# Performance work log

Hardware: AMD Instinct MI355X
Metric: run time of the kernel (lower is better)

The kernel has to match this reference:

```python
import jax, jax.numpy as jnp
import numpy as np

N = 4096   # out_features (rows of W)
M = 4096   # in_features (cols of W)
S_L = 2048 # Givens pairs on rows
S_R = 2048 # Givens pairs on cols
T = 8192   # tokens (batch*seq)
EPS = 1e-6


def _disjoint_pairs(key, n_feat, n_pairs):
    perm = jax.random.permutation(key, n_feat)[: 2 * n_pairs]
    return perm.reshape(n_pairs, 2).astype(jnp.int32)


def setup_inputs() -> dict:
    key = jax.random.key(0)
    ks = jax.random.split(key, 8)
    x = jax.random.normal(ks[0], (T, M), dtype=jnp.float32)
    W = 0.02 * jax.random.normal(ks[1], (N, M), dtype=jnp.float32)
    bias = jnp.zeros((N,), dtype=jnp.float32)
    theta_L = 0.002 * jax.random.normal(ks[2], (S_L,), dtype=jnp.float32)
    theta_R = 0.002 * jax.random.normal(ks[3], (S_R,), dtype=jnp.float32)
    pairs_L = _disjoint_pairs(ks[4], N, S_L)
    pairs_R = _disjoint_pairs(ks[5], M, S_R)
    ecd_log_mag = jnp.zeros((N,), dtype=jnp.float32)
    base_row_norms = jnp.linalg.norm(W, axis=1)  # [N], captured at init
    return {"x": x, "W": W, "bias": bias, "theta_L": theta_L,
            "theta_R": theta_R, "ecd_log_mag": ecd_log_mag,
            "base_row_norms": base_row_norms, "pairs_L": pairs_L,
            "pairs_R": pairs_R}


def _rotate_rows(Wm, pairs, theta):
    # Disjoint Givens rotations on rows: gather pair rows, 2x2 rotate, scatter.
    i, j = pairs[:, 0], pairs[:, 1]
    c = jnp.cos(theta)[:, None]
    s = jnp.sin(theta)[:, None]
    ri, rj = Wm[i], Wm[j]              # [S, M] gathers
    return Wm.at[i].set(c * ri - s * rj).at[j].set(s * ri + c * rj)


def _rotate_cols(Wm, pairs, theta):
    i, j = pairs[:, 0], pairs[:, 1]
    c = jnp.cos(theta)[None, :]
    s = jnp.sin(theta)[None, :]
    ci, cj = Wm[:, i], Wm[:, j]        # [N, S] gathers
    return Wm.at[:, i].set(c * ci - s * cj).at[:, j].set(s * ci + c * cj)


def reference(x, W, bias, theta_L, theta_R, ecd_log_mag, base_row_norms,
              pairs_L, pairs_R):
    # Effective weight: W_eff = G_L(theta_L) @ W @ G_R(theta_R)^T
    W_eff = _rotate_rows(_rotate_cols(W, pairs_R, theta_R), pairs_L, theta_L)
    # Magnitude (ECD) rescaling: restore base per-row norms modulated by
    # learned log-magnitudes.
    row_norms = jnp.sqrt(jnp.sum(W_eff * W_eff, axis=1) + EPS)  # [N]
    scale = base_row_norms * jnp.exp(ecd_log_mag) / row_norms   # [N]
    W_eff = W_eff * scale[:, None]
    return x @ W_eff.T + bias
```

## Files before the change

### kernel.cpp

```cpp
#include <hip/hip_runtime.h>
#include <cstdint>
#include <cstddef>

constexpr int T_N = 8192;
constexpr int MM  = 4096;
constexpr int NN  = 4096;
constexpr int S_L = 2048;
constexpr int S_R = 2048;
constexpr float EPS_ = 1e-6f;

typedef float  f32x4  __attribute__((ext_vector_type(4)));
typedef __bf16 bf16x8 __attribute__((ext_vector_type(8)));
typedef unsigned short ushort8 __attribute__((ext_vector_type(8)));

__device__ __forceinline__ unsigned short f2bf(float f) {
  unsigned int u = __float_as_uint(f);
  u += 0x7FFFu + ((u >> 16) & 1u);
  return (unsigned short)(u >> 16);
}

__global__ void init_maps(float* rowC, float* rowS, int* rowP,
                          float* colC, float* colS, int* colP) {
  int i = blockIdx.x * blockDim.x + threadIdx.x;
  if (i < NN) { rowC[i] = 1.f; rowS[i] = 0.f; rowP[i] = i; }
  if (i < MM) { colC[i] = 1.f; colS[i] = 0.f; colP[i] = i; }
}

__global__ void build_maps(const float* __restrict__ thL, const float* __restrict__ thR,
                           const int* __restrict__ prL, const int* __restrict__ prR,
                           float* rowC, float* rowS, int* rowP,
                           float* colC, float* colS, int* colP) {
  int s = blockIdx.x * blockDim.x + threadIdx.x;
  if (s < S_L) {
    int i = prL[2*s], j = prL[2*s+1];
    float c = cosf(thL[s]), sn = sinf(thL[s]);
    rowC[i] = c; rowS[i] = -sn; rowP[i] = j;
    rowC[j] = c; rowS[j] =  sn; rowP[j] = i;
  }
  if (s < S_R) {
    int i = prR[2*s], j = prR[2*s+1];
    float c = cosf(thR[s]), sn = sinf(thR[s]);
    colC[i] = c; colS[i] = -sn; colP[i] = j;
    colC[j] = c; colS[j] =  sn; colP[j] = i;
  }
}

__global__ __launch_bounds__(256) void build_weff(
    const float* __restrict__ W, const float* __restrict__ brn, const float* __restrict__ elm,
    const float* __restrict__ rowC, const float* __restrict__ rowS, const int* __restrict__ rowP,
    const float* __restrict__ colC, const float* __restrict__ colS, const int* __restrict__ colP,
    unsigned short* __restrict__ Wb)
{
  __shared__ __align__(16) float rA[MM];
  __shared__ __align__(16) float rB[MM];
  __shared__ __align__(16) float rE[MM];
  __shared__ float red[4];

  int n   = blockIdx.x;
  int tid = threadIdx.x;
  int pn  = rowP[n];
  float cl = rowC[n], sl = rowS[n];
  const float* Wn = W + (size_t)n  * MM;
  const float* Wp = W + (size_t)pn * MM;

  for (int m = tid * 4; m < MM; m += 1024) {
    *(f32x4*)&rA[m] = *(const f32x4*)&Wn[m];
    *(f32x4*)&rB[m] = *(const f32x4*)&Wp[m];
  }
  __syncthreads();

  float ss = 0.f;
  for (int m = tid; m < MM; m += 256) {
    int p = colP[m];
    float c = colC[m], s = colS[m];
    float e = cl * (c * rA[m] + s * rA[p]) + sl * (c * rB[m] + s * rB[p]);
    rE[m] = e;
    ss += e * e;
  }
  #pragma unroll
  for (int o = 32; o; o >>= 1) ss += __shfl_xor(ss, o);
  int lane = tid & 63, wid = tid >> 6;
  if (lane == 0) red[wid] = ss;
  __syncthreads();
  float tot = red[0] + red[1] + red[2] + red[3];
  float scale = brn[n] * expf(elm[n]) / sqrtf(tot + EPS_);

  for (int m = tid * 8; m < MM; m += 2048) {
    ushort8 pkt;
    #pragma unroll
    for (int q = 0; q < 8; q++) pkt[q] = f2bf(rE[m + q] * scale);
    *(ushort8*)&Wb[(size_t)n * MM + m] = pkt;
  }
}

__global__ __launch_bounds__(256) void conv_x(const float* __restrict__ x,
                                              unsigned short* __restrict__ xb) {
  const size_t total = (size_t)T_N * MM / 8;
  for (size_t i = (size_t)blockIdx.x * 256 + threadIdx.x; i < total; i += 2048ull * 256ull) {
    const float* s = x + i * 8;
    f32x4 v0 = *(const f32x4*)s;
    f32x4 v1 = *(const f32x4*)(s + 4);
    ushort8 p;
    p[0] = f2bf(v0.x); p[1] = f2bf(v0.y); p[2] = f2bf(v0.z); p[3] = f2bf(v0.w);
    p[4] = f2bf(v1.x); p[5] = f2bf(v1.y); p[6] = f2bf(v1.z); p[7] = f2bf(v1.w);
    *(ushort8*)(xb + i * 8) = p;
  }
}

typedef const __attribute__((address_space(1))) unsigned int* as1_u32p;
typedef __attribute__((address_space(3))) unsigned int* as3_u32p;

__device__ __forceinline__ void gl_lds16(const void* g, void* l) {
  __builtin_amdgcn_global_load_lds((as1_u32p)g, (as3_u32p)l, 16, 0, 0);
}

constexpr int GBM = 256, GBN = 256, GBK = 64;
constexpr int NT = MM / GBK;
constexpr int TILE_BYTES = GBM * GBK * 2;

#define LGKM(N) do { asm volatile("s_waitcnt lgkmcnt(" #N ")" ::: "memory"); \
                     __builtin_amdgcn_sched_barrier(0); } while (0)
#define VMC0()  asm volatile("s_waitcnt vmcnt(0)" ::: "memory")

#define RD_A(DST, AB, Q)                                                      \
  _Pragma("unroll") for (int i_ = 0; i_ < 2; ++i_)                            \
  _Pragma("unroll") for (int kk_ = 0; kk_ < 2; ++kk_)                         \
    DST[i_][kk_] = *(const bf16x8*)((AB) + arow0 + ((Q)*2 + i_) * 2048        \
                                     + ((kk_*64 + lg*16) ^ sw));

#define RD_B(DST, BB)                                                         \
  _Pragma("unroll") for (int ni_ = 0; ni_ < 4; ++ni_)                         \
  _Pragma("unroll") for (int kk_ = 0; kk_ < 2; ++kk_)                         \
    DST[ni_][kk_] = *(const bf16x8*)((BB) + brow0 + ni_ * 2048                \
                                     + ((kk_*64 + lg*16) ^ sw));

#define MFMA_PH(AF, BF, MI0)                                                  \
  __builtin_amdgcn_s_setprio(1);                                              \
  _Pragma("unroll") for (int kk_ = 0; kk_ < 2; ++kk_)                         \
  _Pragma("unroll") for (int i_ = 0; i_ < 2; ++i_)                            \
  _Pragma("unroll") for (int ni_ = 0; ni_ < 4; ++ni_)                         \
    acc[(MI0)+i_][ni_] = __builtin_amdgcn_mfma_f32_16x16x32_bf16(             \
        AF[i_][kk_], BF[ni_][kk_], acc[(MI0)+i_][ni_], 0, 0, 0);              \
  __builtin_amdgcn_s_setprio(0);

#define STAGE(T1)                                                             \
  { const int kof_ = (T1) * GBK;                                              \
    char* dA_ = ldsA + ((T1) & 1) * TILE_BYTES;                               \
    char* dB_ = ldsB + ((T1) & 1) * TILE_BYTES;                               \
    _Pragma("unroll") for (int l_ = 0; l_ < 4; ++l_) {                        \
      gl_lds16(sA + (size_t)l_ * (64 * MM) + kof_, dA_ + dstb + l_ * 8192);   \
      gl_lds16(sB + (size_t)l_ * (64 * MM) + kof_, dB_ + dstb + l_ * 8192);   \
    } }

#define TILE_FULL(T, BFC, BFN, AF0C, AF0N)                                    \
  {                                                                           \
    const int t_ = (T);                                                       \
    const char* Ab_  = ldsA + (t_ & 1) * TILE_BYTES;                          \
    const char* AbN_ = ldsA + ((t_ + 1) & 1) * TILE_BYTES;                    \
    const char* BbN_ = ldsB + ((t_ + 1) & 1) * TILE_BYTES;                    \
    __builtin_amdgcn_s_barrier();                                             \
    STAGE(t_ + 1);                                                            \
    bf16x8 af1[2][2], af2[2][2], af3[2][2];                                   \
    RD_A(af1, Ab_, 1);                                                        \
    LGKM(4);                                                                  \
    MFMA_PH(AF0C, BFC, 0);                                                    \
    RD_A(af2, Ab_, 2);                                                        \
    LGKM(4);                                                                  \
    MFMA_PH(af1, BFC, 2);                                                     \
    RD_A(af3, Ab_, 3);                                                        \
    VMC0();                                                                   \
    __builtin_amdgcn_s_barrier();                                             \
    RD_B(BFN, BbN_);                                                          \
    LGKM(12);                                                                 \
    MFMA_PH(af2, BFC, 4);                                                     \
    RD_A(AF0N, AbN_, 0);                                                      \
    LGKM(12);                                                                 \
    MFMA_PH(af3, BFC, 6);                                                     \
  }

__global__ __launch_bounds__(512, 2) void gemm8(
    const unsigned short* __restrict__ xb,
    const unsigned short* __restrict__ wb,
    const float* __restrict__ bias,
    float* __restrict__ C)
{
  __shared__ __align__(16) unsigned short As[2 * GBM * GBK];
  __shared__ __align__(16) unsigned short Bs[2 * GBN * GBK];
  char* ldsA = (char*)As;
  char* ldsB = (char*)Bs;

  int bid = blockIdx.x;
  int swz = (bid & 7) * 64 + (bid >> 3);
  int tn = swz & 15, tm = swz >> 4;
  const int trow0 = tm * GBM;
  const int tcol0 = tn * GBN;

  int tid  = threadIdx.x;
  int lane = tid & 63;
  int wid  = tid >> 6;
  int wr = wid >> 2, wc = wid & 3;
  int lr = lane & 15;
  int lg = lane >> 4;
  const int sw = (lr & 7) << 4;
  const int arow0 = wr * 16384 + lr * 128;
  const int brow0 = wc * 8192  + lr * 128;

  const int r0   = tid >> 3;
  const int colg = (tid & 7) ^ (r0 & 7);
  const unsigned short* sA = xb + (size_t)(trow0 + r0) * MM + colg * 8;
  const unsigned short* sB = wb + (size_t)(tcol0 + r0) * MM + colg * 8;
  const int dstb = tid * 16;

  f32x4 acc[8][4];
  #pragma unroll
  for (int i = 0; i < 8; i++)
    #pragma unroll
    for (int j = 0; j < 4; j++) {
      f32x4 z = {0.f, 0.f, 0.f, 0.f};
      acc[i][j] = z;
    }

  STAGE(0);
  VMC0();
  __builtin_amdgcn_s_barrier();

  bf16x8 bfA[4][2], bfB[4][2], af0A[2][2], af0B[2][2];
  RD_B(bfA, ldsB);
  RD_A(af0A, ldsA, 0);

  for (int tt = 0; tt < NT - 2; tt += 2) {
    TILE_FULL(tt,     bfA, bfB, af0A, af0B);
    TILE_FULL(tt + 1, bfB, bfA, af0B, af0A);
  }
  TILE_FULL(NT - 2, bfA, bfB, af0A, af0B);

  {
    const char* Ab_ = ldsA + ((NT - 1) & 1) * TILE_BYTES;
    __builtin_amdgcn_s_barrier();
    bf16x8 af1[2][2], af2[2][2], af3[2][2];
    RD_A(af1, Ab_, 1);
    LGKM(4);
    MFMA_PH(af0B, bfB, 0);
    RD_A(af2, Ab_, 2);
    LGKM(4);
    MFMA_PH(af1, bfB, 2);
    RD_A(af3, Ab_, 3);
    LGKM(4);
    MFMA_PH(af2, bfB, 4);
    LGKM(0);
    MFMA_PH(af3, bfB, 6);
  }

  #pragma unroll
  for (int ni = 0; ni < 4; ++ni) {
    int col = tcol0 + wc * 64 + ni * 16 + lr;
    float bi = bias[col];
    #pragma unroll
    for (int mi = 0; mi < 8; ++mi) {
      int rr0 = trow0 + wr * 128 + mi * 16 + lg * 4;
      #pragma unroll
      for (int qq = 0; qq < 4; ++qq)
        C[(size_t)(rr0 + qq) * NN + col] = acc[mi][ni][qq] + bi;
    }
  }
}

constexpr int BM = 128, BN = 128, BK = 64;

__global__ __launch_bounds__(256) void gemm_fb(
    const float* __restrict__ xf,
    const unsigned short* __restrict__ wb, const float* __restrict__ bias,
    float* __restrict__ C)
{
  __shared__ __align__(16) unsigned short As2[BM * BK];
  __shared__ __align__(16) unsigned short Bs2[BN * BK];

  int bid = blockIdx.x;
  int swz = (bid & 7) * 256 + (bid >> 3);
  int tn = swz & 31;
  int tm = swz >> 5;

  int tid  = threadIdx.x;
  int lane = tid & 63;
  int wid  = tid >> 6;
  int wr = wid >> 1, wc = wid & 1;
  int lr = lane & 15;
  int lg = lane >> 4;

  f32x4 acc[4][4];
  #pragma unroll
  for (int i = 0; i < 4; i++)
    #pragma unroll
    for (int j = 0; j < 4; j++) {
      f32x4 z = {0.f, 0.f, 0.f, 0.f};
      acc[i][j] = z;
    }

  int srow = tid >> 3;
  int scol = (tid & 7) * 8;
  const size_t a_base = (size_t)(tm * BM) * MM;
  const size_t b_base = (size_t)(tn * BN) * MM;

  for (int k0 = 0; k0 < MM; k0 += BK) {
    #pragma unroll
    for (int c = 0; c < 4; c++) {
      int row = c * 32 + srow;
      gl_lds16(wb + b_base + (size_t)row * MM + k0 + scol,
               (char*)Bs2 + (c * 256 + wid * 64) * 16);
    }
    #pragma unroll
    for (int c = 0; c < 4; c++) {
      int row = c * 32 + srow;
      const float* s = xf + a_base + (size_t)row * MM + k0 + scol;
      f32x4 v0 = *(const f32x4*)s;
      f32x4 v1 = *(const f32x4*)(s + 4);
      ushort8 p;
      p[0] = f2bf(v0.x); p[1] = f2bf(v0.y); p[2] = f2bf(v0.z); p[3] = f2bf(v0.w);
      p[4] = f2bf(v1.x); p[5] = f2bf(v1.y); p[6] = f2bf(v1.z); p[7] = f2bf(v1.w);
      *(ushort8*)&As2[(c * 256 + tid) * 8] = p;
    }
    __syncthreads();

    #pragma unroll
    for (int kk = 0; kk < 2; kk++) {
      bf16x8 a[4], b[4];
      #pragma unroll
      for (int i = 0; i < 4; i++) {
        a[i] = *(const bf16x8*)&As2[(wr * 64 + i * 16 + lr) * BK + kk * 32 + lg * 8];
        b[i] = *(const bf16x8*)&Bs2[(wc * 64 + i * 16 + lr) * BK + kk * 32 + lg * 8];
      }
      #pragma unroll
      for (int i = 0; i < 4; i++)
        #pragma unroll
        for (int j = 0; j < 4; j++)
          acc[i][j] = __builtin_amdgcn_mfma_f32_16x16x32_bf16(a[i], b[j], acc[i][j], 0, 0, 0);
    }
    __syncthreads();
  }

  int gn0 = tn * BN + wc * 64;
  int gt0 = tm * BM + wr * 64;
  #pragma unroll
  for (int j = 0; j < 4; j++) {
    int gn = gn0 + j * 16 + lr;
    float bi = bias[gn];
    #pragma unroll
    for (int i = 0; i < 4; i++) {
      int t0 = gt0 + i * 16 + lg * 4;
      #pragma unroll
      for (int q = 0; q < 4; q++)
        C[(size_t)(t0 + q) * NN + gn] = acc[i][j][q] + bi;
    }
  }
}

extern "C" void kernel_launch(void* const* d_in, const int* in_sizes, int n_in,
                              void* d_out, int out_size, void* d_ws, size_t ws_size,
                              hipStream_t stream)
{
  const float* x    = (const float*)d_in[0];
  const float* W    = (const float*)d_in[1];
  const float* bias = (const float*)d_in[2];
  const float* thL  = (const float*)d_in[3];
  const float* thR  = (const float*)d_in[4];
  const float* elm  = (const float*)d_in[5];
  const float* brn  = (const float*)d_in[6];
  const int*   prL  = (const int*)d_in[7];
  const int*   prR  = (const int*)d_in[8];
  float* out = (float*)d_out;

  char* ws = (char*)d_ws;
  unsigned short* Wb = (unsigned short*)ws;
  size_t off = (size_t)NN * MM * 2;
  float* rowC = (float*)(ws + off); off += NN * 4;
  float* rowS = (float*)(ws + off); off += NN * 4;
  int*   rowP = (int*)  (ws + off); off += NN * 4;
  float* colC = (float*)(ws + off); off += MM * 4;
  float* colS = (float*)(ws + off); off += MM * 4;
  int*   colP = (int*)  (ws + off); off += MM * 4;
  unsigned short* xb = (unsigned short*)(ws + off);
  bool use_xb = ws_size >= off + (size_t)T_N * MM * 2;

  init_maps <<<16, 256, 0, stream>>>(rowC, rowS, rowP, colC, colS, colP);
  build_maps<<< 8, 256, 0, stream>>>(thL, thR, prL, prR, rowC, rowS, rowP, colC, colS, colP);
  build_weff<<<NN, 256, 0, stream>>>(W, brn, elm, rowC, rowS, rowP, colC, colS, colP, Wb);

  if (use_xb) {
    conv_x<<<2048, 256, 0, stream>>>(x, xb);
    gemm8<<<512, 512, 0, stream>>>(xb, Wb, bias, out);
  } else {
    gemm_fb<<<2048, 256, 0, stream>>>(x, Wb, bias, out);
  }
}
```

Before: 354.5 us.

## Restructure GEMM main loop with triple-buffered A tiles and partial vmcnt gating

Reworks the bf16 GEMM main loop so the A operand is triple-buffered in LDS and prefetched two k-tiles ahead, while B stays double-buffered and is prefetched one tile ahead. Each tile now does one barrier gated on vmcnt(4) instead of a full vmcnt(0) wait plus two barriers. B fragments are read in halves and interleaved with A quarter reads and MFMA clusters. The goal is to hide more global-to-LDS latency and cut synchronisation stalls, at the cost of more LDS per block, which may affect occupancy at 2 blocks per CU.

```diff
diff --git a/kernel.cpp b/kernel.cpp
--- a/kernel.cpp
+++ b/kernel.cpp
@@ -115,67 +115,79 @@
 }
 
 constexpr int GBM = 256, GBN = 256, GBK = 64;
-constexpr int NT = MM / GBK;
-constexpr int TILE_BYTES = GBM * GBK * 2;
-
+constexpr int NTK = MM / GBK;
+constexpr int ASLOT = GBM * GBK * 2;
+constexpr int BSLOT = GBN * GBK * 2;
+
+#define SB0() __builtin_amdgcn_sched_barrier(0)
 #define LGKM(N) do { asm volatile("s_waitcnt lgkmcnt(" #N ")" ::: "memory"); \
-                     __builtin_amdgcn_sched_barrier(0); } while (0)
-#define VMC0()  asm volatile("s_waitcnt vmcnt(0)" ::: "memory")
-
-#define RD_A(DST, AB, Q)                                                      \
+                     SB0(); } while (0)
+
+#define RD_BP(NI0, BB)                                                        \
+  _Pragma("unroll") for (int n_ = 0; n_ < 2; ++n_)                            \
+  _Pragma("unroll") for (int k_ = 0; k_ < 2; ++k_)                            \
+    bf[(NI0) + n_][k_] = *(const bf16x8*)((BB) + brow0 + ((NI0) + n_) * 2048  \
+                                           + ((k_ * 64 + lg * 16) ^ sw));
+
+#define RD_AQ(DST, AB, Q)                                                     \
   _Pragma("unroll") for (int i_ = 0; i_ < 2; ++i_)                            \
-  _Pragma("unroll") for (int kk_ = 0; kk_ < 2; ++kk_)                         \
-    DST[i_][kk_] = *(const bf16x8*)((AB) + arow0 + ((Q)*2 + i_) * 2048        \
-                                     + ((kk_*64 + lg*16) ^ sw));
-
-#define RD_B(DST, BB)                                                         \
-  _Pragma("unroll") for (int ni_ = 0; ni_ < 4; ++ni_)                         \
-  _Pragma("unroll") for (int kk_ = 0; kk_ < 2; ++kk_)                         \
-    DST[ni_][kk_] = *(const bf16x8*)((BB) + brow0 + ni_ * 2048                \
-                                     + ((kk_*64 + lg*16) ^ sw));
-
-#define MFMA_PH(AF, BF, MI0)                                                  \
+  _Pragma("unroll") for (int k_ = 0; k_ < 2; ++k_)                            \
+    DST[i_][k_] = *(const bf16x8*)((AB) + arow0 + ((Q) * 2 + i_) * 2048       \
+                                    + ((k_ * 64 + lg * 16) ^ sw));
+
+#define CL(AF, Q, H)                                                          \
   __builtin_amdgcn_s_setprio(1);                                              \
-  _Pragma("unroll") for (int kk_ = 0; kk_ < 2; ++kk_)                         \
+  _Pragma("unroll") for (int k_ = 0; k_ < 2; ++k_)                            \
   _Pragma("unroll") for (int i_ = 0; i_ < 2; ++i_)                            \
-  _Pragma("unroll") for (int ni_ = 0; ni_ < 4; ++ni_)                         \
-    acc[(MI0)+i_][ni_] = __builtin_amdgcn_mfma_f32_16x16x32_bf16(             \
-        AF[i_][kk_], BF[ni_][kk_], acc[(MI0)+i_][ni_], 0, 0, 0);              \
+  _Pragma("unroll") for (int n_ = 0; n_ < 2; ++n_)                            \
+    acc[(Q) * 2 + i_][(H) + n_] = __builtin_amdgcn_mfma_f32_16x16x32_bf16(    \
+        AF[i_][k_], bf[(H) + n_][k_], acc[(Q) * 2 + i_][(H) + n_], 0, 0, 0);  \
   __builtin_amdgcn_s_setprio(0);
 
-#define STAGE(T1)                                                             \
-  { const int kof_ = (T1) * GBK;                                              \
-    char* dA_ = ldsA + ((T1) & 1) * TILE_BYTES;                               \
-    char* dB_ = ldsB + ((T1) & 1) * TILE_BYTES;                               \
-    _Pragma("unroll") for (int l_ = 0; l_ < 4; ++l_) {                        \
-      gl_lds16(sA + (size_t)l_ * (64 * MM) + kof_, dA_ + dstb + l_ * 8192);   \
-      gl_lds16(sB + (size_t)l_ * (64 * MM) + kof_, dB_ + dstb + l_ * 8192);   \
-    } }
-
-#define TILE_FULL(T, BFC, BFN, AF0C, AF0N)                                    \
+#define STAGE_A(KOF, SL)                                                      \
+  _Pragma("unroll") for (int l_ = 0; l_ < 4; ++l_)                            \
+    gl_lds16(sA + (size_t)l_ * (64 * MM) + (KOF),                             \
+             ldsA + (SL) * ASLOT + dstb + l_ * 8192);
+#define STAGE_B(KOF, SL)                                                      \
+  _Pragma("unroll") for (int l_ = 0; l_ < 4; ++l_)                            \
+    gl_lds16(sB + (size_t)l_ * (64 * MM) + (KOF),                             \
+             ldsB + (SL) * BSLOT + dstb + l_ * 8192);
+
+#define GATE4 do { asm volatile("s_waitcnt vmcnt(4)" ::: "memory");           \
+                   __builtin_amdgcn_s_barrier(); } while (0)
+#define GATE0 do { asm volatile("s_waitcnt vmcnt(0)" ::: "memory");           \
+                   __builtin_amdgcn_s_barrier(); } while (0)
+#define NOGATE do { } while (0)
+
+#define TILE(KOF, RA, RB, WA, WB, DOB, DOA, GATE)                             \
   {                                                                           \
-    const int t_ = (T);                                                       \
-    const char* Ab_  = ldsA + (t_ & 1) * TILE_BYTES;                          \
-    const char* AbN_ = ldsA + ((t_ + 1) & 1) * TILE_BYTES;                    \
-    const char* BbN_ = ldsB + ((t_ + 1) & 1) * TILE_BYTES;                    \
-    __builtin_amdgcn_s_barrier();                                             \
-    STAGE(t_ + 1);                                                            \
-    bf16x8 af1[2][2], af2[2][2], af3[2][2];                                   \
-    RD_A(af1, Ab_, 1);                                                        \
+    const char* Ab_ = ldsA + (RA) * ASLOT;                                    \
+    const char* Bb_ = ldsB + (RB) * BSLOT;                                    \
+    bf16x8 bf[4][2], af0[2][2], af1[2][2], af2[2][2], af3[2][2];              \
+    RD_BP(0, Bb_);                                                            \
+    RD_AQ(af0, Ab_, 0);                                                       \
+    SB0();                                                                    \
+    RD_AQ(af1, Ab_, 1);                                                       \
+    if (DOB) { STAGE_B((KOF) + GBK, WB); }                                    \
+    SB0();                                                                    \
+    if (DOA) { STAGE_A((KOF) + 2 * GBK, WA); }                                \
     LGKM(4);                                                                  \
-    MFMA_PH(AF0C, BFC, 0);                                                    \
-    RD_A(af2, Ab_, 2);                                                        \
+    CL(af0, 0, 0);                                                   \
+    RD_BP(2, Bb_);                                                            \
     LGKM(4);                                                                  \
-    MFMA_PH(af1, BFC, 2);                                                     \
-    RD_A(af3, Ab_, 3);                                                        \
-    VMC0();                                                                   \
-    __builtin_amdgcn_s_barrier();                                             \
-    RD_B(BFN, BbN_);                                                          \
-    LGKM(12);                                                                 \
-    MFMA_PH(af2, BFC, 4);                                                     \
-    RD_A(AF0N, AbN_, 0);                                                      \
-    LGKM(12);                                                                 \
-    MFMA_PH(af3, BFC, 6);                                                     \
+    CL(af1, 1, 0);                                                   \
+    RD_AQ(af2, Ab_, 2);                                                       \
+    LGKM(4);                                                                  \
+    CL(af0, 0, 2);                                                   \
+    RD_AQ(af3, Ab_, 3);                                                       \
+    LGKM(4);                                                                  \
+    CL(af1, 1, 2);                                                   \
+    CL(af2, 2, 0);                                                   \
+    CL(af2, 2, 2);                                                   \
+    LGKM(0);                                                                  \
+    CL(af3, 3, 0);                                                   \
+    CL(af3, 3, 2);                                                   \
+    GATE;                                                                     \
   }
 
 __global__ __launch_bounds__(512, 2) void gemm8(
@@ -184,7 +196,7 @@
     const float* __restrict__ bias,
     float* __restrict__ C)
 {
-  __shared__ __align__(16) unsigned short As[2 * GBM * GBK];
+  __shared__ __align__(16) unsigned short As[3 * GBM * GBK];
   __shared__ __align__(16) unsigned short Bs[2 * GBN * GBK];
   char* ldsA = (char*)As;
   char* ldsB = (char*)Bs;
@@ -220,36 +232,30 @@
       acc[i][j] = z;
     }
 
-  STAGE(0);
-  VMC0();
+  STAGE_B(0, 0);
+  STAGE_A(0, 0);
+  SB0();
+  STAGE_B(GBK, 1);
+  STAGE_A(GBK, 1);
+  STAGE_A(2 * GBK, 2);
+  asm volatile("s_waitcnt vmcnt(12)" ::: "memory");
   __builtin_amdgcn_s_barrier();
 
-  bf16x8 bfA[4][2], bfB[4][2], af0A[2][2], af0B[2][2];
-  RD_B(bfA, ldsB);
-  RD_A(af0A, ldsA, 0);
-
-  for (int tt = 0; tt < NT - 2; tt += 2) {
-    TILE_FULL(tt,     bfA, bfB, af0A, af0B);
-    TILE_FULL(tt + 1, bfB, bfA, af0B, af0A);
-  }
-  TILE_FULL(NT - 2, bfA, bfB, af0A, af0B);
-
-  {
-    const char* Ab_ = ldsA + ((NT - 1) & 1) * TILE_BYTES;
-    __builtin_amdgcn_s_barrier();
-    bf16x8 af1[2][2], af2[2][2], af3[2][2];
-    RD_A(af1, Ab_, 1);
-    LGKM(4);
-    MFMA_PH(af0B, bfB, 0);
-    RD_A(af2, Ab_, 2);
-    LGKM(4);
-    MFMA_PH(af1, bfB, 2);
-    RD_A(af3, Ab_, 3);
-    LGKM(4);
-    MFMA_PH(af2, bfB, 4);
-    LGKM(0);
-    MFMA_PH(af3, bfB, 6);
-  }
+  int kof = 0;
+  #pragma unroll 1
+  for (int tb = 0; tb < NTK - 4; tb += 6) {
+    TILE(kof      , 0, 0, 2, 1, 1, 1, GATE4);
+    TILE(kof +  64, 1, 1, 0, 0, 1, 1, GATE4);
+    TILE(kof + 128, 2, 0, 1, 1, 1, 1, GATE4);
+    TILE(kof + 192, 0, 1, 2, 0, 1, 1, GATE4);
+    TILE(kof + 256, 1, 0, 0, 1, 1, 1, GATE4);
+    TILE(kof + 320, 2, 1, 1, 0, 1, 1, GATE4);
+    kof += 384;
+  }
+  TILE(kof      , 0, 0, 2, 1, 1, 1, GATE4);
+  TILE(kof +  64, 1, 1, 0, 0, 1, 1, GATE4);
+  TILE(kof + 128, 2, 0, 0, 1, 1, 0, GATE0);
+  TILE(kof + 192, 0, 1, 0, 0, 0, 0, NOGATE);
 
   #pragma unroll
   for (int ni = 0; ni < 4; ++ni) {
```

After: 325.4 us. 1.09x faster.
